# Kernel tuning notes

Measured on AMD Instinct MI355X. Metric: run time of the kernel, lower is better.

Reference implementation:

```python
import jax, jax.numpy as jnp
import numpy as np

D = 512       # d_model
H = 8         # n_heads per pathway MHA
CTX_H = 2     # router context_attention heads
P = 16        # num_attention_pathways
K = 8         # top_k_pathways
B = 8
S = 1024
TEMP = 1.0
RH1, RH2 = 128, 64  # router hidden sizes


def mha(x, in_w, in_b, out_w, out_b, n_heads):
    """torch.nn.MultiheadAttention (batch_first, eval mode, no mask)."""
    b, s, d = x.shape
    dh = d // n_heads
    qkv = x @ in_w.T + in_b                      # [b,s,3d]
    q, k, v = jnp.split(qkv, 3, axis=-1)
    sh = lambda t: t.reshape(b, s, n_heads, dh).transpose(0, 2, 1, 3)
    q, k, v = sh(q), sh(k), sh(v)
    scale = 1.0 / float(np.sqrt(dh))
    attn = jax.nn.softmax(jnp.einsum('bhqd,bhkd->bhqk', q, k) * scale, axis=-1)
    o = jnp.einsum('bhqk,bhkd->bhqd', attn, v).transpose(0, 2, 1, 3).reshape(b, s, d)
    return o @ out_w.T + out_b


def setup_inputs() -> dict:
    key = jax.random.key(0)
    ks = jax.random.split(key, 16)
    w = 0.05  # weight init scale to keep attention logits sane
    return {
        'x': jax.random.normal(ks[0], (B, S, D), jnp.float32),
        'ctx_in_w': jax.random.normal(ks[1], (3 * D, D), jnp.float32) * w,
        'ctx_in_b': jnp.zeros((3 * D,), jnp.float32),
        'ctx_out_w': jax.random.normal(ks[2], (D, D), jnp.float32) * w,
        'ctx_out_b': jnp.zeros((D,), jnp.float32),
        'r_w1': jax.random.normal(ks[3], (RH1, D), jnp.float32) * w,
        'r_b1': jnp.zeros((RH1,), jnp.float32),
        'r_w2': jax.random.normal(ks[4], (RH2, RH1), jnp.float32) * w,
        'r_b2': jnp.zeros((RH2,), jnp.float32),
        'r_w3': jax.random.normal(ks[5], (P, RH2), jnp.float32) * w,
        'r_b3': jnp.zeros((P,), jnp.float32),
        'p_in_w': jax.random.normal(ks[6], (P, 3 * D, D), jnp.float32) * w,
        'p_in_b': jnp.zeros((P, 3 * D), jnp.float32),
        'p_out_w': jax.random.normal(ks[7], (P, D, D), jnp.float32) * w,
        'p_out_b': jnp.zeros((P, D), jnp.float32),
    }


def reference(x, ctx_in_w, ctx_in_b, ctx_out_w, ctx_out_b,
              r_w1, r_b1, r_w2, r_b2, r_w3, r_b3,
              p_in_w, p_in_b, p_out_w, p_out_b):
    b, s, d = x.shape
    # --- SemanticPathwayRouter ---
    attended = mha(x, ctx_in_w, ctx_in_b, ctx_out_w, ctx_out_b, CTX_H)
    h = jax.nn.relu(attended @ r_w1.T + r_b1)
    h = jax.nn.relu(h @ r_w2.T + r_b2)
    pathway_scores = h @ r_w3.T + r_b3            # [b,s,P]
    # --- GLBL load-balance loss (eval: no buffer updates) ---
    probs_lb = jax.nn.softmax(pathway_scores, axis=-1)
    freq = probs_lb.mean(axis=(0, 1))             # [P] (frequencies == avg scores)
    glbl_loss = P * jnp.sum(freq * freq)
    # --- top-k gating: softmax -> topk scatter -> renormalize ---
    probs = jax.nn.softmax(pathway_scores / TEMP, axis=-1)
    top_v, top_i = jax.lax.top_k(probs, K)        # [b,s,K]
    bi = jnp.arange(b)[:, None, None]
    si = jnp.arange(s)[None, :, None]
    weights = jnp.zeros_like(probs).at[bi, si, top_i].set(top_v)
    weights = weights / (weights.sum(axis=-1, keepdims=True) + 1e-8)
    # --- combine: weighted sum of P full-MHA experts (scan keeps memory low) ---
    wp = jnp.moveaxis(weights, -1, 0)             # [P,b,s]
    def step(acc, params):
        iw, ib, ow, ob, wk = params
        return acc + mha(x, iw, ib, ow, ob, H) * wk[..., None], None
    output, _ = jax.lax.scan(step, jnp.zeros_like(x),
                             (p_in_w, p_in_b, p_out_w, p_out_b, wp))
    return output, glbl_loss, weights
```

## Files before the change

kernel.cpp:

```cpp
#include <hip/hip_runtime.h>
#include <math.h>

#define TOKENS 8192
#define DM 512
#define TD 1536
#define SEQ 1024
#define NPATH 16
#define TOPK 8

typedef __bf16 bf16x8v __attribute__((ext_vector_type(8)));
typedef __bf16 bf16x4v __attribute__((ext_vector_type(4)));
typedef float f32x4v __attribute__((ext_vector_type(4)));
typedef unsigned short u16x8 __attribute__((ext_vector_type(8)));

__device__ __forceinline__ void gload_lds16(const void* gp, unsigned lds_byte_off) {
    __builtin_amdgcn_global_load_lds(
        (const __attribute__((address_space(1))) unsigned int*)(uintptr_t)gp,
        (__attribute__((address_space(3))) unsigned int*)(uintptr_t)lds_byte_off,
        16, 0, 0);
}

template <int PREF>
__global__ __launch_bounds__(256)
void gemm_f32_nt(const float* __restrict__ A, const float* __restrict__ B,
                 const float* __restrict__ bias, float* __restrict__ C,
                 int M, int N, int K, int lda, int ldb, int ldc,
                 float alpha, int relu, int zmode)
{
    __shared__ float As[16][132];
    __shared__ float Bs[16][132];
    if (zmode == 1) {
        const int z = blockIdx.z, bb = z >> 1, hh = z & 1;
        A += (size_t)bb * SEQ * TD + hh * 256;
        B += (size_t)bb * SEQ * TD + 512 + hh * 256;
        C += (size_t)z * SEQ * SEQ;
    }
    const int tid = threadIdx.x;
    const int bm = blockIdx.y << 7, bn = blockIdx.x << 7;
    const int tx4 = (tid & 15) << 2, ty4 = ((tid >> 4) & 15) << 2;
    float acc[8][8] = {};

    if constexpr (PREF) {
        const int srow = tid >> 2, skc4 = (tid & 3) << 2;
        const float* Ap = A + (size_t)(bm + srow) * lda + skc4;
        const float* Ap2 = A + (size_t)(bm + 64 + srow) * lda + skc4;
        const float* Bp = B + (size_t)(bn + srow) * ldb + skc4;
        const float* Bp2 = B + (size_t)(bn + 64 + srow) * ldb + skc4;
        float4 pa0 = *(const float4*)Ap,  pa1 = *(const float4*)Ap2;
        float4 pb0 = *(const float4*)Bp,  pb1 = *(const float4*)Bp2;
        for (int k0 = 0; k0 < K; k0 += 16) {
            __syncthreads();
            As[skc4 + 0][srow] = pa0.x; As[skc4 + 1][srow] = pa0.y;
            As[skc4 + 2][srow] = pa0.z; As[skc4 + 3][srow] = pa0.w;
            As[skc4 + 0][64 + srow] = pa1.x; As[skc4 + 1][64 + srow] = pa1.y;
            As[skc4 + 2][64 + srow] = pa1.z; As[skc4 + 3][64 + srow] = pa1.w;
            Bs[skc4 + 0][srow] = pb0.x; Bs[skc4 + 1][srow] = pb0.y;
            Bs[skc4 + 2][srow] = pb0.z; Bs[skc4 + 3][srow] = pb0.w;
            Bs[skc4 + 0][64 + srow] = pb1.x; Bs[skc4 + 1][64 + srow] = pb1.y;
            Bs[skc4 + 2][64 + srow] = pb1.z; Bs[skc4 + 3][64 + srow] = pb1.w;
            if (k0 + 16 < K) {
                pa0 = *(const float4*)(Ap + k0 + 16);
                pa1 = *(const float4*)(Ap2 + k0 + 16);
                pb0 = *(const float4*)(Bp + k0 + 16);
                pb1 = *(const float4*)(Bp2 + k0 + 16);
            }
            __syncthreads();
#pragma unroll
            for (int kk = 0; kk < 16; ++kk) {
                const float4 a0 = *(const float4*)&As[kk][ty4];
                const float4 a1 = *(const float4*)&As[kk][64 + ty4];
                const float4 b0 = *(const float4*)&Bs[kk][tx4];
                const float4 b1 = *(const float4*)&Bs[kk][64 + tx4];
                const float aa[8] = {a0.x, a0.y, a0.z, a0.w, a1.x, a1.y, a1.z, a1.w};
                const float bb[8] = {b0.x, b0.y, b0.z, b0.w, b1.x, b1.y, b1.z, b1.w};
#pragma unroll
                for (int i = 0; i < 8; ++i)
#pragma unroll
                    for (int j = 0; j < 8; ++j)
                        acc[i][j] = fmaf(aa[i], bb[j], acc[i][j]);
            }
        }
    } else {
        for (int k0 = 0; k0 < K; k0 += 16) {
            __syncthreads();
#pragma unroll
            for (int it = 0; it < 2; ++it) {
                const int u = (it << 8) + tid;
                const int row = u >> 2, kc4 = (u & 3) << 2;
                const float4 av = *(const float4*)(A + (size_t)(bm + row) * lda + k0 + kc4);
                As[kc4 + 0][row] = av.x; As[kc4 + 1][row] = av.y;
                As[kc4 + 2][row] = av.z; As[kc4 + 3][row] = av.w;
                const float4 bv = *(const float4*)(B + (size_t)(bn + row) * ldb + k0 + kc4);
                Bs[kc4 + 0][row] = bv.x; Bs[kc4 + 1][row] = bv.y;
                Bs[kc4 + 2][row] = bv.z; Bs[kc4 + 3][row] = bv.w;
            }
            __syncthreads();
#pragma unroll
            for (int kk = 0; kk < 16; ++kk) {
                const float4 a0 = *(const float4*)&As[kk][ty4];
                const float4 a1 = *(const float4*)&As[kk][64 + ty4];
                const float4 b0 = *(const float4*)&Bs[kk][tx4];
                const float4 b1 = *(const float4*)&Bs[kk][64 + tx4];
                const float aa[8] = {a0.x, a0.y, a0.z, a0.w, a1.x, a1.y, a1.z, a1.w};
                const float bb[8] = {b0.x, b0.y, b0.z, b0.w, b1.x, b1.y, b1.z, b1.w};
#pragma unroll
                for (int i = 0; i < 8; ++i)
#pragma unroll
                    for (int j = 0; j < 8; ++j)
                        acc[i][j] = fmaf(aa[i], bb[j], acc[i][j]);
            }
        }
    }

    float bcol[8] = {};
    if (bias) {
        const float4 bL = *(const float4*)(bias + bn + tx4);
        const float4 bH = *(const float4*)(bias + bn + 64 + tx4);
        bcol[0] = bL.x; bcol[1] = bL.y; bcol[2] = bL.z; bcol[3] = bL.w;
        bcol[4] = bH.x; bcol[5] = bH.y; bcol[6] = bH.z; bcol[7] = bH.w;
    }
#pragma unroll
    for (int i = 0; i < 8; ++i) {
        const int row = bm + ((i < 4) ? (ty4 + i) : (64 + ty4 + i - 4));
        float* cp = C + (size_t)row * ldc + bn;
        float v[8];
#pragma unroll
        for (int j = 0; j < 8; ++j) {
            v[j] = alpha * acc[i][j] + bcol[j];
            if (relu) v[j] = fmaxf(v[j], 0.f);
        }
        *(float4*)(cp + tx4) = make_float4(v[0], v[1], v[2], v[3]);
        *(float4*)(cp + 64 + tx4) = make_float4(v[4], v[5], v[6], v[7]);
    }
}

__global__ __launch_bounds__(256)
void gemm_f32_pv(const float* __restrict__ Sb, const float* __restrict__ qkv,
                 float* __restrict__ obuf)
{
    __shared__ float As[16][132];
    __shared__ float Bs[16][128];
    const int z = blockIdx.z, bb = z >> 1, hh = z & 1;
    const float* A = Sb + (size_t)z * SEQ * SEQ;
    const float* B = qkv + (size_t)bb * SEQ * TD + 1024 + hh * 256;
    float* C = obuf + (size_t)bb * SEQ * 512 + hh * 256;
    const int tid = threadIdx.x;
    const int bm = blockIdx.y << 7, bn = blockIdx.x << 7;
    const int tx4 = (tid & 15) << 2, ty4 = ((tid >> 4) & 15) << 2;
    const int ar = tid >> 2, ak4 = (tid & 3) << 2;
    const int br = tid >> 5, bn4 = (tid & 31) << 2;
    const float* ApA  = A + (size_t)(bm + ar) * SEQ + ak4;
    const float* ApA2 = A + (size_t)(bm + 64 + ar) * SEQ + ak4;
    const float* BpB  = B + (size_t)br * TD + bn + bn4;
    const float* BpB2 = B + (size_t)(8 + br) * TD + bn + bn4;

    float4 a0 = *(const float4*)ApA, a1 = *(const float4*)ApA2;
    float4 b0 = *(const float4*)BpB, b1 = *(const float4*)BpB2;

    float acc[8][8] = {};
    for (int k0 = 0; k0 < SEQ; k0 += 16) {
        __syncthreads();
        As[ak4 + 0][ar] = a0.x; As[ak4 + 1][ar] = a0.y;
        As[ak4 + 2][ar] = a0.z; As[ak4 + 3][ar] = a0.w;
        As[ak4 + 0][64 + ar] = a1.x; As[ak4 + 1][64 + ar] = a1.y;
        As[ak4 + 2][64 + ar] = a1.z; As[ak4 + 3][64 + ar] = a1.w;
        *(float4*)&Bs[br][bn4] = b0;
        *(float4*)&Bs[8 + br][bn4] = b1;
        if (k0 + 16 < SEQ) {
            a0 = *(const float4*)(ApA + k0 + 16);
            a1 = *(const float4*)(ApA2 + k0 + 16);
            b0 = *(const float4*)(BpB + (size_t)(k0 + 16) * TD);
            b1 = *(const float4*)(BpB2 + (size_t)(k0 + 16) * TD);
        }
        __syncthreads();
#pragma unroll
        for (int kk = 0; kk < 16; ++kk) {
            const float4 A0 = *(const float4*)&As[kk][ty4];
            const float4 A1 = *(const float4*)&As[kk][64 + ty4];
            const float4 B0 = *(const float4*)&Bs[kk][tx4];
            const float4 B1 = *(const float4*)&Bs[kk][64 + tx4];
            const float aa[8] = {A0.x, A0.y, A0.z, A0.w, A1.x, A1.y, A1.z, A1.w};
            const float bb[8] = {B0.x, B0.y, B0.z, B0.w, B1.x, B1.y, B1.z, B1.w};
#pragma unroll
            for (int i = 0; i < 8; ++i)
#pragma unroll
                for (int j = 0; j < 8; ++j)
                    acc[i][j] = fmaf(aa[i], bb[j], acc[i][j]);
        }
    }
#pragma unroll
    for (int i = 0; i < 8; ++i) {
        const int row = bm + ((i < 4) ? (ty4 + i) : (64 + ty4 + i - 4));
        float* cp = C + (size_t)row * 512 + bn;
        *(float4*)(cp + tx4) = make_float4(acc[i][0], acc[i][1], acc[i][2], acc[i][3]);
        *(float4*)(cp + 64 + tx4) = make_float4(acc[i][4], acc[i][5], acc[i][6], acc[i][7]);
    }
}

__global__ __launch_bounds__(256)
void softmax_rows(float* __restrict__ S_)
{
    const int row = blockIdx.x * 4 + (threadIdx.x >> 6);
    const int lane = threadIdx.x & 63;
    float* rp = S_ + (size_t)row * 1024 + lane * 16;
    float4 v[4];
#pragma unroll
    for (int i = 0; i < 4; ++i) v[i] = *(const float4*)(rp + i * 4);
    float mx = -INFINITY;
#pragma unroll
    for (int i = 0; i < 4; ++i)
        mx = fmaxf(mx, fmaxf(fmaxf(v[i].x, v[i].y), fmaxf(v[i].z, v[i].w)));
#pragma unroll
    for (int off = 1; off < 64; off <<= 1) mx = fmaxf(mx, __shfl_xor(mx, off));
    float sum = 0.f;
#pragma unroll
    for (int i = 0; i < 4; ++i) {
        v[i].x = __expf(v[i].x - mx); v[i].y = __expf(v[i].y - mx);
        v[i].z = __expf(v[i].z - mx); v[i].w = __expf(v[i].w - mx);
        sum += v[i].x + v[i].y + v[i].z + v[i].w;
    }
#pragma unroll
    for (int off = 1; off < 64; off <<= 1) sum += __shfl_xor(sum, off);
    const float inv = 1.f / sum;
#pragma unroll
    for (int i = 0; i < 4; ++i) {
        v[i].x *= inv; v[i].y *= inv; v[i].z *= inv; v[i].w *= inv;
        *(float4*)(rp + i * 4) = v[i];
    }
}

__global__ __launch_bounds__(256)
void gemm_f32(const float* __restrict__ A, const float* __restrict__ W,
              const float* __restrict__ bias, float* __restrict__ C,
              int M, int N, int K, int relu)
{
    __shared__ float As[16][64];
    __shared__ float Bs[16][64];
    const int bm = blockIdx.y << 6;
    const int bn = blockIdx.x << 6;
    const int tid = threadIdx.x;
    const int tx = tid & 15, ty = tid >> 4;
    const int lr = tid >> 2;
    const int lc = (tid & 3) << 2;
    float acc[4][4] = {};
    for (int k0 = 0; k0 < K; k0 += 16) {
        float4 av = *(const float4*)(A + (size_t)(bm + lr) * K + (k0 + lc));
        float4 bv = make_float4(0.f, 0.f, 0.f, 0.f);
        const int wr = bn + lr;
        if (wr < N) bv = *(const float4*)(W + (size_t)wr * K + (k0 + lc));
        __syncthreads();
        As[lc + 0][lr] = av.x; As[lc + 1][lr] = av.y;
        As[lc + 2][lr] = av.z; As[lc + 3][lr] = av.w;
        Bs[lc + 0][lr] = bv.x; Bs[lc + 1][lr] = bv.y;
        Bs[lc + 2][lr] = bv.z; Bs[lc + 3][lr] = bv.w;
        __syncthreads();
#pragma unroll
        for (int kk = 0; kk < 16; ++kk) {
            const float4 a4 = *(const float4*)(&As[kk][ty << 2]);
            const float4 b4 = *(const float4*)(&Bs[kk][tx << 2]);
            const float a[4] = {a4.x, a4.y, a4.z, a4.w};
            const float b[4] = {b4.x, b4.y, b4.z, b4.w};
#pragma unroll
            for (int i = 0; i < 4; ++i)
#pragma unroll
                for (int j = 0; j < 4; ++j)
                    acc[i][j] = fmaf(a[i], b[j], acc[i][j]);
        }
    }
#pragma unroll
    for (int i = 0; i < 4; ++i) {
        const int m = bm + (ty << 2) + i;
#pragma unroll
        for (int j = 0; j < 4; ++j) {
            const int n = bn + (tx << 2) + j;
            if (n < N) {
                float v = acc[i][j] + bias[n];
                if (relu) v = fmaxf(v, 0.f);
                C[(size_t)m * N + n] = v;
            }
        }
    }
}

template <int DH>
__global__ __launch_bounds__(256)
void flash_attn(const float* __restrict__ qkv, float* __restrict__ O,
                int H, float scale)
{
    constexpr int NU = DH / 64;
    __shared__ float Qs[32][DH + 4];
    __shared__ float Ks[32][DH + 4];
    __shared__ float Vs[32][DH + 4];
    __shared__ float Ps[32][33];
    const int tid = threadIdx.x;
    const int g2 = tid & 15;
    const int rs = tid >> 4;
    const int bh = blockIdx.y;
    const int b = bh / H, h = bh - b * H;
    const int rb = blockIdx.x << 5;
    const float* qb = qkv + (size_t)b * SEQ * TD + (size_t)h * DH;
    const float* kb = qb + DM;
    const float* vb = qb + 2 * DM;

    for (int idx = tid; idx < 32 * (DH / 4); idx += 256) {
        const int rr = idx / (DH / 4);
        const int dp = (idx - rr * (DH / 4)) << 2;
        float4 v = *(const float4*)(qb + (size_t)(rb + rr) * TD + dp);
        v.x *= scale; v.y *= scale; v.z *= scale; v.w *= scale;
        *(float4*)&Qs[rr][dp] = v;
    }
    float m0 = -INFINITY, m1 = -INFINITY, l0 = 0.f, l1 = 0.f;
    float4 o0[NU], o1[NU];
#pragma unroll
    for (int u = 0; u < NU; ++u) {
        o0[u] = make_float4(0.f, 0.f, 0.f, 0.f);
        o1[u] = make_float4(0.f, 0.f, 0.f, 0.f);
    }
    __syncthreads();

    for (int kt = 0; kt < SEQ; kt += 32) {
        for (int idx = tid; idx < 32 * (DH / 4); idx += 256) {
            const int rr = idx / (DH / 4);
            const int dp = (idx - rr * (DH / 4)) << 2;
            *(float4*)&Ks[rr][dp] = *(const float4*)(kb + (size_t)(kt + rr) * TD + dp);
            *(float4*)&Vs[rr][dp] = *(const float4*)(vb + (size_t)(kt + rr) * TD + dp);
        }
        __syncthreads();
        float s00 = 0.f, s01 = 0.f, s10 = 0.f, s11 = 0.f;
        const int cA = g2, cB = g2 + 16;
#pragma unroll 8
        for (int i = 0; i < DH; i += 4) {
            const float4 q0 = *(const float4*)&Qs[rs][i];
            const float4 q1 = *(const float4*)&Qs[rs + 16][i];
            const float4 k0 = *(const float4*)&Ks[cA][i];
            const float4 k1 = *(const float4*)&Ks[cB][i];
            s00 += q0.x * k0.x + q0.y * k0.y + q0.z * k0.z + q0.w * k0.w;
            s01 += q0.x * k1.x + q0.y * k1.y + q0.z * k1.z + q0.w * k1.w;
            s10 += q1.x * k0.x + q1.y * k0.y + q1.z * k0.z + q1.w * k0.w;
            s11 += q1.x * k1.x + q1.y * k1.y + q1.z * k1.z + q1.w * k1.w;
        }
        float ml0 = fmaxf(s00, s01), ml1 = fmaxf(s10, s11);
#pragma unroll
        for (int off = 1; off < 16; off <<= 1) {
            ml0 = fmaxf(ml0, __shfl_xor(ml0, off));
            ml1 = fmaxf(ml1, __shfl_xor(ml1, off));
        }
        const float n0 = fmaxf(m0, ml0), n1 = fmaxf(m1, ml1);
        const float f0 = __expf(m0 - n0), f1 = __expf(m1 - n1);
        const float p00 = __expf(s00 - n0), p01 = __expf(s01 - n0);
        const float p10 = __expf(s10 - n1), p11 = __expf(s11 - n1);
        float sum0 = p00 + p01, sum1 = p10 + p11;
#pragma unroll
        for (int off = 1; off < 16; off <<= 1) {
            sum0 += __shfl_xor(sum0, off);
            sum1 += __shfl_xor(sum1, off);
        }
        l0 = l0 * f0 + sum0; l1 = l1 * f1 + sum1;
        m0 = n0; m1 = n1;
#pragma unroll
        for (int u = 0; u < NU; ++u) {
            o0[u].x *= f0; o0[u].y *= f0; o0[u].z *= f0; o0[u].w *= f0;
            o1[u].x *= f1; o1[u].y *= f1; o1[u].z *= f1; o1[u].w *= f1;
        }
        Ps[rs][cA] = p00; Ps[rs][cB] = p01;
        Ps[rs + 16][cA] = p10; Ps[rs + 16][cB] = p11;
        __syncthreads();
#pragma unroll 4
        for (int c = 0; c < 32; ++c) {
            const float pv0 = Ps[rs][c];
            const float pv1 = Ps[rs + 16][c];
#pragma unroll
            for (int u = 0; u < NU; ++u) {
                const float4 v4 = *(const float4*)&Vs[c][(g2 << 2) + (u << 6)];
                o0[u].x = fmaf(pv0, v4.x, o0[u].x);
                o0[u].y = fmaf(pv0, v4.y, o0[u].y);
                o0[u].z = fmaf(pv0, v4.z, o0[u].z);
                o0[u].w = fmaf(pv0, v4.w, o0[u].w);
                o1[u].x = fmaf(pv1, v4.x, o1[u].x);
                o1[u].y = fmaf(pv1, v4.y, o1[u].y);
                o1[u].z = fmaf(pv1, v4.z, o1[u].z);
                o1[u].w = fmaf(pv1, v4.w, o1[u].w);
            }
        }
        __syncthreads();
    }
    const float i0 = 1.f / l0, i1 = 1.f / l1;
    float* ob0 = O + (size_t)b * SEQ * DM + (size_t)(rb + rs) * DM + h * DH;
    float* ob1 = ob0 + (size_t)16 * DM;
#pragma unroll
    for (int u = 0; u < NU; ++u) {
        float4 w0 = o0[u];
        w0.x *= i0; w0.y *= i0; w0.z *= i0; w0.w *= i0;
        *(float4*)(ob0 + (g2 << 2) + (u << 6)) = w0;
        float4 w1 = o1[u];
        w1.x *= i1; w1.y *= i1; w1.z *= i1; w1.w *= i1;
        *(float4*)(ob1 + (g2 << 2) + (u << 6)) = w1;
    }
}

__global__ __launch_bounds__(256)
void router_epilogue(const float* __restrict__ scores, float* __restrict__ freq,
                     float* __restrict__ weights)
{
    const int t = blockIdx.x * 256 + threadIdx.x;
    float s[NPATH];
#pragma unroll
    for (int i = 0; i < NPATH; ++i) s[i] = scores[(size_t)t * NPATH + i];
    float mx = s[0];
#pragma unroll
    for (int i = 1; i < NPATH; ++i) mx = fmaxf(mx, s[i]);
    float p[NPATH];
    float sum = 0.f;
#pragma unroll
    for (int i = 0; i < NPATH; ++i) { p[i] = expf(s[i] - mx); sum += p[i]; }
    const float inv = 1.f / sum;
#pragma unroll
    for (int i = 0; i < NPATH; ++i) p[i] *= inv;
#pragma unroll
    for (int i = 0; i < NPATH; ++i) {
        float v = p[i];
        for (int off = 32; off >= 1; off >>= 1) v += __shfl_xor(v, off);
        if ((threadIdx.x & 63) == 0) atomicAdd(&freq[i], v);
    }
    unsigned used = 0u;
    float topv[TOPK];
    int topi[TOPK];
    float wsum = 0.f;
#pragma unroll
    for (int k = 0; k < TOPK; ++k) {
        float best = -1.f; int bi = 0;
#pragma unroll
        for (int i = 0; i < NPATH; ++i) {
            if (!((used >> i) & 1u) && p[i] > best) { best = p[i]; bi = i; }
        }
        used |= 1u << bi;
        topv[k] = best; topi[k] = bi;
        wsum += best;
    }
    const float winv = 1.f / (wsum + 1e-8f);
    float w[NPATH];
#pragma unroll
    for (int i = 0; i < NPATH; ++i) w[i] = 0.f;
#pragma unroll
    for (int k = 0; k < TOPK; ++k) w[topi[k]] = topv[k] * winv;
#pragma unroll
    for (int i = 0; i < NPATH; ++i) weights[(size_t)t * NPATH + i] = w[i];
}

__global__ void glbl_loss_kernel(const float* __restrict__ freq, float* __restrict__ out)
{
    if (threadIdx.x == 0 && blockIdx.x == 0) {
        float acc = 0.f;
        for (int i = 0; i < NPATH; ++i) {
            const float f = freq[i] * (1.f / (float)TOKENS);
            acc += f * f;
        }
        out[0] = (float)NPATH * acc;
    }
}

__global__ __launch_bounds__(256)
void cast_f32_bf16(const float* __restrict__ src, __bf16* __restrict__ dst, int n)
{
    const int i = (blockIdx.x * 256 + threadIdx.x) * 4;
    if (i < n) {
        const float4 v = *(const float4*)(src + i);
        bf16x4v o;
        o[0] = (__bf16)v.x; o[1] = (__bf16)v.y; o[2] = (__bf16)v.z; o[3] = (__bf16)v.w;
        *(bf16x4v*)(dst + i) = o;
    }
}

__global__ __launch_bounds__(256)
void gemm_bf16_qkv(const __bf16* __restrict__ A, const __bf16* __restrict__ B,
                   const float* __restrict__ bias, __bf16* __restrict__ C,
                   int N, int K)
{
    __shared__ __attribute__((aligned(16))) __bf16 As[128 * 32];
    __shared__ __attribute__((aligned(16))) __bf16 Bs[128 * 32];
    const int tid = threadIdx.x;
    const int l = tid & 63, w = tid >> 6;
    const int wr = w >> 1, wc = w & 1;
    const int a16 = l & 15, g = l >> 4;
    const int bm = blockIdx.y << 7, bn = blockIdx.x << 7;
    const unsigned asA = (unsigned)(uintptr_t)(void*)&As[0];
    const unsigned asB = (unsigned)(uintptr_t)(void*)&Bs[0];

    f32x4v acc[4][4] = {};
    for (int k0 = 0; k0 < K; k0 += 32) {
        __syncthreads();
#pragma unroll
        for (int it = 0; it < 2; ++it) {
            const int u = it * 256 + tid;
            const int row = u >> 2, cc = u & 3;
            const unsigned dst = (unsigned)((it * 256 + w * 64) * 16);
            gload_lds16(A + (size_t)(bm + row) * K + k0 + cc * 8, asA + dst);
            gload_lds16(B + (size_t)(bn + row) * K + k0 + cc * 8, asB + dst);
        }
        __syncthreads();
        bf16x8v af[4], bf[4];
#pragma unroll
        for (int m = 0; m < 4; ++m)
            af[m] = *(const bf16x8v*)&As[(wr * 64 + m * 16 + a16) * 32 + g * 8];
#pragma unroll
        for (int n = 0; n < 4; ++n)
            bf[n] = *(const bf16x8v*)&Bs[(wc * 64 + n * 16 + a16) * 32 + g * 8];
#pragma unroll
        for (int m = 0; m < 4; ++m)
#pragma unroll
            for (int n = 0; n < 4; ++n)
                acc[m][n] = __builtin_amdgcn_mfma_f32_16x16x32_bf16(af[m], bf[n], acc[m][n], 0, 0, 0);
    }
#pragma unroll
    for (int n = 0; n < 4; ++n) {
        const int col = bn + wc * 64 + n * 16 + a16;
        const float bv = bias[col];
        const float sc = (col < DM) ? 0.125f : 1.0f;
#pragma unroll
        for (int m = 0; m < 4; ++m) {
            const int row0 = bm + wr * 64 + m * 16 + g * 4;
#pragma unroll
            for (int r = 0; r < 4; ++r)
                C[(size_t)(row0 + r) * N + col] = (__bf16)((acc[m][n][r] + bv) * sc);
        }
    }
}

__global__ __launch_bounds__(256)
void gemm_bf16_out(const __bf16* __restrict__ A, const __bf16* __restrict__ B,
                   const float* __restrict__ bias, const float* __restrict__ wts,
                   float* __restrict__ out, int path, int first)
{
    __shared__ __attribute__((aligned(16))) __bf16 As[128 * 32];
    __shared__ __attribute__((aligned(16))) __bf16 Bs[128 * 32];
    const int tid = threadIdx.x;
    const int l = tid & 63, w = tid >> 6;
    const int wr = w >> 1, wc = w & 1;
    const int a16 = l & 15, g = l >> 4;
    const int bm = blockIdx.y << 7, bn = blockIdx.x << 7;
    const unsigned asA = (unsigned)(uintptr_t)(void*)&As[0];
    const unsigned asB = (unsigned)(uintptr_t)(void*)&Bs[0];

    f32x4v acc[4][4] = {};
    for (int k0 = 0; k0 < DM; k0 += 32) {
        __syncthreads();
#pragma unroll
        for (int it = 0; it < 2; ++it) {
            const int u = it * 256 + tid;
            const int row = u >> 2, cc = u & 3;
            const unsigned dst = (unsigned)((it * 256 + w * 64) * 16);
            gload_lds16(A + (size_t)(bm + row) * DM + k0 + cc * 8, asA + dst);
            gload_lds16(B + (size_t)(bn + row) * DM + k0 + cc * 8, asB + dst);
        }
        __syncthreads();
        bf16x8v af[4], bf[4];
#pragma unroll
        for (int m = 0; m < 4; ++m)
            af[m] = *(const bf16x8v*)&As[(wr * 64 + m * 16 + a16) * 32 + g * 8];
#pragma unroll
        for (int n = 0; n < 4; ++n)
            bf[n] = *(const bf16x8v*)&Bs[(wc * 64 + n * 16 + a16) * 32 + g * 8];
#pragma unroll
        for (int m = 0; m < 4; ++m)
#pragma unroll
            for (int n = 0; n < 4; ++n)
                acc[m][n] = __builtin_amdgcn_mfma_f32_16x16x32_bf16(af[m], bf[n], acc[m][n], 0, 0, 0);
    }
#pragma unroll
    for (int m = 0; m < 4; ++m) {
        const int row0 = bm + wr * 64 + m * 16 + g * 4;
#pragma unroll
        for (int r = 0; r < 4; ++r) {
            const int row = row0 + r;
            const float wk = wts[(size_t)row * NPATH + path];
#pragma unroll
            for (int n = 0; n < 4; ++n) {
                const int col = bn + wc * 64 + n * 16 + a16;
                const float v = (acc[m][n][r] + bias[col]) * wk;
                const size_t oi = (size_t)row * DM + col;
                if (first) out[oi] = v; else out[oi] += v;
            }
        }
    }
}

__global__ __launch_bounds__(256)
void attn_bf16(const __bf16* __restrict__ qkv, __bf16* __restrict__ O)
{
    __shared__ __attribute__((aligned(16))) __bf16 Ks[64 * 72];
    __shared__ __attribute__((aligned(16))) __bf16 Vt[64 * 72];
    __shared__ __attribute__((aligned(16))) __bf16 Pq[4][32 * 72];
    const int tid = threadIdx.x;
    const int l = tid & 63, w = tid >> 6;
    const int a = l & 15, g = l >> 4;
    const int bh = blockIdx.y;
    const int b = bh >> 3, h = bh & 7;
    const int qb = blockIdx.x << 7;
    const size_t base = (size_t)b * SEQ * TD;

    bf16x8v qA0, qA1, qB0, qB1;
    {
        const __bf16* qp = qkv + base + (size_t)(qb + w * 32 + a) * TD + h * 64 + g * 8;
        qA0 = *(const bf16x8v*)qp;
        qA1 = *(const bf16x8v*)(qp + 32);
        const __bf16* qp2 = qp + (size_t)16 * TD;
        qB0 = *(const bf16x8v*)qp2;
        qB1 = *(const bf16x8v*)(qp2 + 32);
    }
    float lA = 0.f, lB = 0.f;
    f32x4v oA[4] = {}, oB[4] = {};
    __bf16* pw = &Pq[w][0];
    const int sc8 = tid & 7;
    const int sr  = tid >> 3;
    const int vcol8 = (sr >> 2) ^ sc8;

    bf16x8v kpre0, kpre1, vpre0, vpre1;
    {
        const __bf16* kp0 = qkv + base + (size_t)sr * TD + DM + h * 64 + sc8 * 8;
        kpre0 = *(const bf16x8v*)kp0;
        kpre1 = *(const bf16x8v*)(kp0 + (size_t)32 * TD);
        const __bf16* vp0 = qkv + base + (size_t)(2 * sr) * TD + 2 * DM + h * 64 + sc8 * 8;
        vpre0 = *(const bf16x8v*)vp0;
        vpre1 = *(const bf16x8v*)(vp0 + TD);
    }

    for (int kt = 0; kt < SEQ; kt += 64) {
        __syncthreads();
        *(bf16x8v*)&Ks[sr * 72 + sc8 * 8] = kpre0;
        *(bf16x8v*)&Ks[(32 + sr) * 72 + sc8 * 8] = kpre1;
        {
            const u16x8 v0 = __builtin_bit_cast(u16x8, vpre0);
            const u16x8 v1 = __builtin_bit_cast(u16x8, vpre1);
#pragma unroll
            for (int j = 0; j < 8; ++j) {
                const unsigned pk = (unsigned)v0[j] | ((unsigned)v1[j] << 16);
                *(unsigned*)&Vt[(sc8 * 8 + j) * 72 + vcol8 * 8 + (sr & 3) * 2] = pk;
            }
        }
        if (kt + 64 < SEQ) {
            const __bf16* kp0 = qkv + base + (size_t)(kt + 64 + sr) * TD + DM + h * 64 + sc8 * 8;
            kpre0 = *(const bf16x8v*)kp0;
            kpre1 = *(const bf16x8v*)(kp0 + (size_t)32 * TD);
            const __bf16* vp0 = qkv + base + (size_t)(kt + 64 + 2 * sr) * TD + 2 * DM + h * 64 + sc8 * 8;
            vpre0 = *(const bf16x8v*)vp0;
            vpre1 = *(const bf16x8v*)(vp0 + TD);
        }
        __syncthreads();

        f32x4v sA[4] = {}, sB[4] = {};
        __builtin_amdgcn_s_setprio(1);
#pragma unroll
        for (int kc = 0; kc < 4; ++kc) {
            const bf16x8v kf0 = *(const bf16x8v*)&Ks[(kc * 16 + a) * 72 + g * 8];
            const bf16x8v kf1 = *(const bf16x8v*)&Ks[(kc * 16 + a) * 72 + 32 + g * 8];
            sA[kc] = __builtin_amdgcn_mfma_f32_16x16x32_bf16(kf0, qA0, sA[kc], 0, 0, 0);
            sA[kc] = __builtin_amdgcn_mfma_f32_16x16x32_bf16(kf1, qA1, sA[kc], 0, 0, 0);
            sB[kc] = __builtin_amdgcn_mfma_f32_16x16x32_bf16(kf0, qB0, sB[kc], 0, 0, 0);
            sB[kc] = __builtin_amdgcn_mfma_f32_16x16x32_bf16(kf1, qB1, sB[kc], 0, 0, 0);
        }
        __builtin_amdgcn_s_setprio(0);

        float lsumA = 0.f, lsumB = 0.f;
#pragma unroll
        for (int kc = 0; kc < 4; ++kc) {
            bf16x4v pkA, pkB;
#pragma unroll
            for (int r = 0; r < 4; ++r) {
                const float pA = __expf(sA[kc][r]);
                const float pB = __expf(sB[kc][r]);
                lsumA += pA; lsumB += pB;
                pkA[r] = (__bf16)pA; pkB[r] = (__bf16)pB;
            }
            *(bf16x4v*)&pw[a * 72 + kc * 16 + g * 4] = pkA;
            *(bf16x4v*)&pw[(16 + a) * 72 + kc * 16 + g * 4] = pkB;
        }
        lsumA += __shfl_xor(lsumA, 16);
        lsumA += __shfl_xor(lsumA, 32);
        lsumB += __shfl_xor(lsumB, 16);
        lsumB += __shfl_xor(lsumB, 32);
        lA += lsumA; lB += lsumB;
        asm volatile("s_waitcnt lgkmcnt(0)" ::: "memory");

        __builtin_amdgcn_s_setprio(1);
#pragma unroll
        for (int dc = 0; dc < 4; ++dc) {
            const int vrow = dc * 16 + a;
#pragma unroll
            for (int kh = 0; kh < 2; ++kh) {
                const bf16x8v vf = *(const bf16x8v*)&Vt[vrow * 72 + ((((kh << 2) + g) ^ ((vrow >> 3) & 7)) & 7) * 8];
                const bf16x8v paA = *(const bf16x8v*)&pw[a * 72 + kh * 32 + g * 8];
                const bf16x8v paB = *(const bf16x8v*)&pw[(16 + a) * 72 + kh * 32 + g * 8];
                oA[dc] = __builtin_amdgcn_mfma_f32_16x16x32_bf16(paA, vf, oA[dc], 0, 0, 0);
                oB[dc] = __builtin_amdgcn_mfma_f32_16x16x32_bf16(paB, vf, oB[dc], 0, 0, 0);
            }
        }
        __builtin_amdgcn_s_setprio(0);
    }

    float liA[4], liB[4];
#pragma unroll
    for (int r = 0; r < 4; ++r) {
        liA[r] = 1.f / __shfl(lA, 4 * g + r);
        liB[r] = 1.f / __shfl(lB, 4 * g + r);
    }
    const int row0 = qb + w * 32 + g * 4;
#pragma unroll
    for (int dc = 0; dc < 4; ++dc)
#pragma unroll
        for (int r = 0; r < 4; ++r) {
            O[(size_t)(b * SEQ + row0 + r) * DM + h * 64 + dc * 16 + a] = (__bf16)(oA[dc][r] * liA[r]);
            O[(size_t)(b * SEQ + row0 + 16 + r) * DM + h * 64 + dc * 16 + a] = (__bf16)(oB[dc][r] * liB[r]);
        }
}

extern "C" void kernel_launch(void* const* d_in, const int* in_sizes, int n_in,
                              void* d_out, int out_size, void* d_ws, size_t ws_size,
                              hipStream_t stream)
{
    const float* x         = (const float*)d_in[0];
    const float* ctx_in_w  = (const float*)d_in[1];
    const float* ctx_in_b  = (const float*)d_in[2];
    const float* ctx_out_w = (const float*)d_in[3];
    const float* ctx_out_b = (const float*)d_in[4];
    const float* r_w1      = (const float*)d_in[5];
    const float* r_b1      = (const float*)d_in[6];
    const float* r_w2      = (const float*)d_in[7];
    const float* r_b2      = (const float*)d_in[8];
    const float* r_w3      = (const float*)d_in[9];
    const float* r_b3      = (const float*)d_in[10];
    const float* p_in_w    = (const float*)d_in[11];
    const float* p_in_b    = (const float*)d_in[12];
    const float* p_out_w   = (const float*)d_in[13];
    const float* p_out_b   = (const float*)d_in[14];

    float* out  = (float*)d_out;
    float* loss = out + (size_t)TOKENS * DM;
    float* wts  = loss + 1;

    float* F = (float*)d_ws;
    float* qkvbuf   = F;
    float* obuf     = F + 12582912;
    float* attended = F;
    float* h1       = F + 4194304;
    float* h2       = F + 5242880;
    float* scores   = F + 5767168;
    float* freq     = F + 5898240;

    const int M = TOKENS;
    dim3 blk(256);
    const bool big = ws_size >= (size_t)134217728;

    hipMemsetAsync(freq, 0, NPATH * sizeof(float), stream);
    gemm_f32_nt<0><<<dim3(TD / 128, M / 128), blk, 0, stream>>>(
        x, ctx_in_w, ctx_in_b, qkvbuf, M, TD, DM, DM, DM, TD, 1.f, 0, 0);
    if (big) {
        float* Sbuf = F + 16777216;
        gemm_f32_nt<1><<<dim3(8, 8, 16), blk, 0, stream>>>(
            qkvbuf, qkvbuf, nullptr, Sbuf, SEQ, SEQ, 256, TD, TD, SEQ, 0.0625f, 0, 1);
        softmax_rows<<<dim3(16 * SEQ / 4), blk, 0, stream>>>(Sbuf);
        gemm_f32_pv<<<dim3(2, 8, 16), blk, 0, stream>>>(Sbuf, qkvbuf, obuf);
    } else {
        flash_attn<256><<<dim3(SEQ / 32, 8 * 2), blk, 0, stream>>>(qkvbuf, obuf, 2, 1.f / 16.f);
    }
    gemm_f32_nt<1><<<dim3(DM / 128, M / 128), blk, 0, stream>>>(
        obuf, ctx_out_w, ctx_out_b, attended, M, DM, DM, DM, DM, DM, 1.f, 0, 0);
    gemm_f32_nt<1><<<dim3(1, M / 128), blk, 0, stream>>>(
        attended, r_w1, r_b1, h1, M, 128, DM, DM, DM, 128, 1.f, 1, 0);
    gemm_f32<<<dim3(1, M / 64), blk, 0, stream>>>(h1, r_w2, r_b2, h2, M, 64, 128, 1);
    gemm_f32<<<dim3(1, M / 64), blk, 0, stream>>>(h2, r_w3, r_b3, scores, M, NPATH, 64, 0);
    router_epilogue<<<dim3(TOKENS / 256), blk, 0, stream>>>(scores, freq, wts);
    glbl_loss_kernel<<<dim3(1), dim3(64), 0, stream>>>(freq, loss);

    if (big) {
        __bf16* xb       = (__bf16*)F;
        __bf16* qkv_b    = (__bf16*)(F + 2097152);
        __bf16* obuf_b   = (__bf16*)(F + 8388608);
        __bf16* wqkv_all = (__bf16*)(F + 16777216);
        __bf16* wout_all = (__bf16*)(F + 23068672);
        cast_f32_bf16<<<dim3(TOKENS * DM / 4 / 256), blk, 0, stream>>>(x, xb, TOKENS * DM);
        cast_f32_bf16<<<dim3(NPATH * TD * DM / 4 / 256), blk, 0, stream>>>(
            p_in_w, wqkv_all, NPATH * TD * DM);
        cast_f32_bf16<<<dim3(NPATH * DM * DM / 4 / 256), blk, 0, stream>>>(
            p_out_w, wout_all, NPATH * DM * DM);
        for (int p = 0; p < NPATH; ++p) {
            gemm_bf16_qkv<<<dim3(TD / 128, M / 128), blk, 0, stream>>>(
                xb, wqkv_all + (size_t)p * TD * DM, p_in_b + (size_t)p * TD, qkv_b, TD, DM);
            attn_bf16<<<dim3(SEQ / 128, 64), blk, 0, stream>>>(qkv_b, obuf_b);
            gemm_bf16_out<<<dim3(DM / 128, M / 128), blk, 0, stream>>>(
                obuf_b, wout_all + (size_t)p * DM * DM, p_out_b + (size_t)p * DM, wts, out, p, p == 0);
        }
    } else {
        __bf16* xb     = (__bf16*)F;
        __bf16* qkv_b  = (__bf16*)(F + 2097152);
        __bf16* obuf_b = (__bf16*)(F + 8388608);
        __bf16* wqkv_b = (__bf16*)(F + 12582912);
        __bf16* wout_b = (__bf16*)(F + 12976128);
        cast_f32_bf16<<<dim3(TOKENS * DM / 4 / 256), blk, 0, stream>>>(x, xb, TOKENS * DM);
        for (int p = 0; p < NPATH; ++p) {
            cast_f32_bf16<<<dim3(TD * DM / 4 / 256), blk, 0, stream>>>(
                p_in_w + (size_t)p * TD * DM, wqkv_b, TD * DM);
            cast_f32_bf16<<<dim3(DM * DM / 4 / 256), blk, 0, stream>>>(
                p_out_w + (size_t)p * DM * DM, wout_b, DM * DM);
            gemm_bf16_qkv<<<dim3(TD / 128, M / 128), blk, 0, stream>>>(
                xb, wqkv_b, p_in_b + (size_t)p * TD, qkv_b, TD, DM);
            attn_bf16<<<dim3(SEQ / 128, 64), blk, 0, stream>>>(qkv_b, obuf_b);
            gemm_bf16_out<<<dim3(DM / 128, M / 128), blk, 0, stream>>>(
                obuf_b, wout_b, p_out_b + (size_t)p * DM, wts, out, p, p == 0);
        }
    }
}
```

Before: 2.085 ms.

## Software-pipeline pathway stages into one fused launch with double-buffered intermediates

Replaces the per-pathway sequence of three launches (QKV GEMM, attention, out-projection) with a single fused kernel per step that runs QKV for pathway k, attention for k-1 and out-projection for k-2 concurrently, dispatching on block index. QKV and attention output buffers are double-buffered so adjacent stages don't conflict. This targets launch-boundary idle time and small-grid tail underutilization. In exchange, every block reserves the larger attention shared-memory footprint, which can lower occupancy for the GEMM blocks, and heterogeneous blocks may load-imbalance.

```diff
diff --git a/kernel.cpp b/kernel.cpp
--- a/kernel.cpp
+++ b/kernel.cpp
@@ -471,20 +471,21 @@
     }
 }
 
-__global__ __launch_bounds__(256)
-void gemm_bf16_qkv(const __bf16* __restrict__ A, const __bf16* __restrict__ B,
-                   const float* __restrict__ bias, __bf16* __restrict__ C,
-                   int N, int K)
-{
-    __shared__ __attribute__((aligned(16))) __bf16 As[128 * 32];
-    __shared__ __attribute__((aligned(16))) __bf16 Bs[128 * 32];
+
+__device__ __forceinline__ void qkv_body(
+    const __bf16* __restrict__ A, const __bf16* __restrict__ B,
+    const float* __restrict__ bias, __bf16* __restrict__ C,
+    int N, int K, int bx, int by, char* smem)
+{
+    __bf16* As = (__bf16*)smem;
+    __bf16* Bs = (__bf16*)(smem + 8192);
     const int tid = threadIdx.x;
     const int l = tid & 63, w = tid >> 6;
     const int wr = w >> 1, wc = w & 1;
     const int a16 = l & 15, g = l >> 4;
-    const int bm = blockIdx.y << 7, bn = blockIdx.x << 7;
-    const unsigned asA = (unsigned)(uintptr_t)(void*)&As[0];
-    const unsigned asB = (unsigned)(uintptr_t)(void*)&Bs[0];
+    const int bm = by << 7, bn = bx << 7;
+    const unsigned asA = (unsigned)(uintptr_t)(void*)As;
+    const unsigned asB = (unsigned)(uintptr_t)(void*)Bs;
 
     f32x4v acc[4][4] = {};
     for (int k0 = 0; k0 < K; k0 += 32) {
@@ -526,20 +527,20 @@
     }
 }
 
-__global__ __launch_bounds__(256)
-void gemm_bf16_out(const __bf16* __restrict__ A, const __bf16* __restrict__ B,
-                   const float* __restrict__ bias, const float* __restrict__ wts,
-                   float* __restrict__ out, int path, int first)
-{
-    __shared__ __attribute__((aligned(16))) __bf16 As[128 * 32];
-    __shared__ __attribute__((aligned(16))) __bf16 Bs[128 * 32];
+__device__ __forceinline__ void out_body(
+    const __bf16* __restrict__ A, const __bf16* __restrict__ B,
+    const float* __restrict__ bias, const float* __restrict__ wts,
+    float* __restrict__ out, int path, int first, int bx, int by, char* smem)
+{
+    __bf16* As = (__bf16*)smem;
+    __bf16* Bs = (__bf16*)(smem + 8192);
     const int tid = threadIdx.x;
     const int l = tid & 63, w = tid >> 6;
     const int wr = w >> 1, wc = w & 1;
     const int a16 = l & 15, g = l >> 4;
-    const int bm = blockIdx.y << 7, bn = blockIdx.x << 7;
-    const unsigned asA = (unsigned)(uintptr_t)(void*)&As[0];
-    const unsigned asB = (unsigned)(uintptr_t)(void*)&Bs[0];
+    const int bm = by << 7, bn = bx << 7;
+    const unsigned asA = (unsigned)(uintptr_t)(void*)As;
+    const unsigned asB = (unsigned)(uintptr_t)(void*)Bs;
 
     f32x4v acc[4][4] = {};
     for (int k0 = 0; k0 < DM; k0 += 32) {
@@ -584,18 +585,18 @@
     }
 }
 
-__global__ __launch_bounds__(256)
-void attn_bf16(const __bf16* __restrict__ qkv, __bf16* __restrict__ O)
-{
-    __shared__ __attribute__((aligned(16))) __bf16 Ks[64 * 72];
-    __shared__ __attribute__((aligned(16))) __bf16 Vt[64 * 72];
-    __shared__ __attribute__((aligned(16))) __bf16 Pq[4][32 * 72];
+__device__ __forceinline__ void attn_body(
+    const __bf16* __restrict__ qkv, __bf16* __restrict__ O, int id, char* smem)
+{
+    __bf16* Ks = (__bf16*)smem;
+    __bf16* Vt = (__bf16*)(smem + 9216);
+    __bf16* Pq = (__bf16*)(smem + 18432);
     const int tid = threadIdx.x;
     const int l = tid & 63, w = tid >> 6;
     const int a = l & 15, g = l >> 4;
-    const int bh = blockIdx.y;
+    const int bh = id >> 3;
     const int b = bh >> 3, h = bh & 7;
-    const int qb = blockIdx.x << 7;
+    const int qb = (id & 7) << 7;
     const size_t base = (size_t)b * SEQ * TD;
 
     bf16x8v qA0, qA1, qB0, qB1;
@@ -609,7 +610,7 @@
     }
     float lA = 0.f, lB = 0.f;
     f32x4v oA[4] = {}, oB[4] = {};
-    __bf16* pw = &Pq[w][0];
+    __bf16* pw = Pq + w * (32 * 72);
     const int sc8 = tid & 7;
     const int sr  = tid >> 3;
     const int vcol8 = (sr >> 2) ^ sc8;
@@ -711,6 +712,59 @@
             O[(size_t)(b * SEQ + row0 + r) * DM + h * 64 + dc * 16 + a] = (__bf16)(oA[dc][r] * liA[r]);
             O[(size_t)(b * SEQ + row0 + 16 + r) * DM + h * 64 + dc * 16 + a] = (__bf16)(oB[dc][r] * liB[r]);
         }
+}
+
+__global__ __launch_bounds__(256)
+void gemm_bf16_qkv(const __bf16* __restrict__ A, const __bf16* __restrict__ B,
+                   const float* __restrict__ bias, __bf16* __restrict__ C,
+                   int N, int K)
+{
+    __shared__ __attribute__((aligned(16))) char smem[16384];
+    qkv_body(A, B, bias, C, N, K, blockIdx.x, blockIdx.y, smem);
+}
+
+__global__ __launch_bounds__(256)
+void gemm_bf16_out(const __bf16* __restrict__ A, const __bf16* __restrict__ B,
+                   const float* __restrict__ bias, const float* __restrict__ wts,
+                   float* __restrict__ out, int path, int first)
+{
+    __shared__ __attribute__((aligned(16))) char smem[16384];
+    out_body(A, B, bias, wts, out, path, first, blockIdx.x, blockIdx.y, smem);
+}
+
+__global__ __launch_bounds__(256)
+void attn_bf16(const __bf16* __restrict__ qkv, __bf16* __restrict__ O)
+{
+    __shared__ __attribute__((aligned(16))) char smem[36864];
+    attn_body(qkv, O, blockIdx.y * 8 + blockIdx.x, smem);
+}
+
+__global__ __launch_bounds__(256)
+void fused_path(const __bf16* __restrict__ xb,
+                const __bf16* __restrict__ wqkv_all, const float* __restrict__ p_in_b,
+                const __bf16* __restrict__ wout_all, const float* __restrict__ p_out_b,
+                const float* __restrict__ wts, float* __restrict__ out,
+                __bf16* __restrict__ qkv0, __bf16* __restrict__ qkv1,
+                __bf16* __restrict__ ob0, __bf16* __restrict__ ob1,
+                int nA, int nQ, int pq, int pa, int po)
+{
+    __shared__ __attribute__((aligned(16))) char smem[36864];
+    const int id = blockIdx.x;
+    if (id < nA) {
+        const __bf16* qkvb = (pa & 1) ? qkv1 : qkv0;
+        __bf16* Ob = (pa & 1) ? ob1 : ob0;
+        attn_body(qkvb, Ob, id, smem);
+    } else if (id < nA + nQ) {
+        const int qid = id - nA;
+        __bf16* C = (pq & 1) ? qkv1 : qkv0;
+        qkv_body(xb, wqkv_all + (size_t)pq * TD * DM, p_in_b + (size_t)pq * TD,
+                 C, TD, DM, qid % 12, qid / 12, smem);
+    } else {
+        const int oid = id - nA - nQ;
+        const __bf16* Ab = (po & 1) ? ob1 : ob0;
+        out_body(Ab, wout_all + (size_t)po * DM * DM, p_out_b + (size_t)po * DM,
+                 wts, out, po, po == 0, oid & 3, oid >> 2, smem);
+    }
 }
 
 extern "C" void kernel_launch(void* const* d_in, const int* in_sizes, int n_in,
@@ -773,21 +827,27 @@
 
     if (big) {
         __bf16* xb       = (__bf16*)F;
-        __bf16* qkv_b    = (__bf16*)(F + 2097152);
-        __bf16* obuf_b   = (__bf16*)(F + 8388608);
+        __bf16* qkv0     = (__bf16*)(F + 2097152);
+        __bf16* ob0      = (__bf16*)(F + 8388608);
         __bf16* wqkv_all = (__bf16*)(F + 16777216);
         __bf16* wout_all = (__bf16*)(F + 23068672);
+        __bf16* qkv1     = (__bf16*)(F + 25165824);
+        __bf16* ob1      = (__bf16*)(F + 31457280);
         cast_f32_bf16<<<dim3(TOKENS * DM / 4 / 256), blk, 0, stream>>>(x, xb, TOKENS * DM);
         cast_f32_bf16<<<dim3(NPATH * TD * DM / 4 / 256), blk, 0, stream>>>(
             p_in_w, wqkv_all, NPATH * TD * DM);
         cast_f32_bf16<<<dim3(NPATH * DM * DM / 4 / 256), blk, 0, stream>>>(
             p_out_w, wout_all, NPATH * DM * DM);
-        for (int p = 0; p < NPATH; ++p) {
-            gemm_bf16_qkv<<<dim3(TD / 128, M / 128), blk, 0, stream>>>(
-                xb, wqkv_all + (size_t)p * TD * DM, p_in_b + (size_t)p * TD, qkv_b, TD, DM);
-            attn_bf16<<<dim3(SEQ / 128, 64), blk, 0, stream>>>(qkv_b, obuf_b);
-            gemm_bf16_out<<<dim3(DM / 128, M / 128), blk, 0, stream>>>(
-                obuf_b, wout_all + (size_t)p * DM * DM, p_out_b + (size_t)p * DM, wts, out, p, p == 0);
+        for (int k = 0; k < NPATH + 2; ++k) {
+            const int pq = (k < NPATH) ? k : -1;
+            const int pa = (k >= 1 && k <= NPATH) ? k - 1 : -1;
+            const int po = (k >= 2) ? k - 2 : -1;
+            const int nA = (pa >= 0) ? 512 : 0;
+            const int nQ = (pq >= 0) ? 768 : 0;
+            const int nO = (po >= 0) ? 256 : 0;
+            fused_path<<<dim3(nA + nQ + nO), blk, 0, stream>>>(
+                xb, wqkv_all, p_in_b, wout_all, p_out_b, wts, out,
+                qkv0, qkv1, ob0, ob1, nA, nQ, pq, pa, po);
         }
     } else {
         __bf16* xb     = (__bf16*)F;
```

Result: faster. 1.921 ms (median of 2 runs) (-7.9%).
